# Kernel optimization log

Measured on AMD Instinct MI355X. Metric: run time of the kernel, lower is better.

## Reference

```python
import jax, jax.numpy as jnp
import numpy as np

L, B, D = 2048, 8, 1024
EPS = 1e-5


def setup_inputs() -> dict:
    key = jax.random.key(0)
    k1, k2 = jax.random.split(key)
    x = jax.random.normal(k1, (L, B, D), dtype=jnp.float32)
    c = jnp.zeros((B, D), dtype=jnp.float32)
    # w_ufr: Linear(D, 3D); weight init normal(std=0.001), bias zero except
    # the reset-gate third which is filled with 2.0 (per the torch init).
    W = jax.random.normal(k2, (3 * D, D), dtype=jnp.float32) * 0.001
    b = jnp.zeros((3 * D,), dtype=jnp.float32).at[2 * D:].set(2.0)
    gamma = jnp.ones((D,), dtype=jnp.float32)
    beta = jnp.zeros((D,), dtype=jnp.float32)
    return {"x": x, "c": c, "W": W, "b": b, "gamma": gamma, "beta": beta}


def _layernorm(x, gamma, beta):
    mu = jnp.mean(x, axis=-1, keepdims=True)
    var = jnp.var(x, axis=-1, keepdims=True)
    return (x - mu) * jax.lax.rsqrt(var + EPS) * gamma + beta


def reference(x, c, W, b, gamma, beta):
    residual = x
    x_norm = _layernorm(x, gamma, beta)            # [L,B,D]
    ufr = jnp.einsum('lbd,ed->lbe', x_norm, W) + b  # [L,B,3D]
    u, f, r = jnp.split(ufr, 3, axis=-1)
    f_gate = jax.nn.sigmoid(f)
    r_gate = jax.nn.sigmoid(r)

    def step(c_prev, fu):
        f_t, u_t = fu
        c_t = f_t * c_prev + (1.0 - f_t) * u_t
        return c_t, c_t

    last_c, c_stack = jax.lax.scan(step, c, (f_gate, u))  # c_stack: [L,B,D]
    hs = r_gate * jnp.tanh(c_stack) + (1.0 - r_gate) * x_norm
    # dropout is identity in eval mode
    return residual + hs, last_c
```

## Files before the change

### kernel.cpp

```cpp
#include <hip/hip_runtime.h>
#include <hip/hip_bf16.h>

#define L_DIM 2048
#define B_DIM 8
#define D_DIM 1024
#define M_DIM (L_DIM * B_DIM)
#define N_DIM (3 * D_DIM)
#define K_DIM D_DIM
#define BD (B_DIM * D_DIM)
#define NCHUNK 64
#define CLEN (L_DIM / NCHUNK)

typedef __attribute__((ext_vector_type(8))) __bf16 bf16x8;
typedef __attribute__((ext_vector_type(4))) __bf16 bf16x4;
typedef __attribute__((ext_vector_type(4))) float f32x4;

#define GLOAD_LDS16(g, l)                                        \
  __builtin_amdgcn_global_load_lds(                              \
      (const __attribute__((address_space(1))) void*)(g),        \
      (__attribute__((address_space(3))) void*)(l), 16, 0, 0)

__device__ __forceinline__ float sigmoidf_(float v) {
  return 1.0f / (1.0f + __expf(-v));
}

__global__ __launch_bounds__(256) void ln_kernel(
    const float* __restrict__ x, const float* __restrict__ gamma,
    const float* __restrict__ beta, __bf16* __restrict__ xn,
    float* __restrict__ muA, float* __restrict__ rsA) {
  const int row = blockIdx.x;
  const int tid = threadIdx.x;
  const float4 v = ((const float4*)(x + (size_t)row * D_DIM))[tid];
  float s  = v.x + v.y + v.z + v.w;
  float ss = v.x * v.x + v.y * v.y + v.z * v.z + v.w * v.w;
  #pragma unroll
  for (int off = 32; off > 0; off >>= 1) {
    s  += __shfl_xor(s, off);
    ss += __shfl_xor(ss, off);
  }
  __shared__ float sb[8];
  const int wid = tid >> 6, lane = tid & 63;
  if (lane == 0) { sb[wid] = s; sb[4 + wid] = ss; }
  __syncthreads();
  const float tot  = sb[0] + sb[1] + sb[2] + sb[3];
  const float tot2 = sb[4] + sb[5] + sb[6] + sb[7];
  const float mu  = tot * (1.0f / D_DIM);
  const float var = tot2 * (1.0f / D_DIM) - mu * mu;
  const float rstd = rsqrtf(var + 1e-5f);
  if (tid == 0) { muA[row] = mu; rsA[row] = rstd; }
  const float4 g  = ((const float4*)gamma)[tid];
  const float4 bt = ((const float4*)beta)[tid];
  bf16x4 o;
  o[0] = (__bf16)((v.x - mu) * rstd * g.x + bt.x);
  o[1] = (__bf16)((v.y - mu) * rstd * g.y + bt.y);
  o[2] = (__bf16)((v.z - mu) * rstd * g.z + bt.z);
  o[3] = (__bf16)((v.w - mu) * rstd * g.w + bt.w);
  ((bf16x4*)(xn + (size_t)row * D_DIM))[tid] = o;
}

__global__ __launch_bounds__(256) void wconv_kernel(
    const float* __restrict__ W, __bf16* __restrict__ Wb) {
  const size_t i = ((size_t)blockIdx.x * 256 + threadIdx.x) * 4;
  const float4 v = *(const float4*)(W + i);
  bf16x4 o;
  o[0] = (__bf16)v.x; o[1] = (__bf16)v.y; o[2] = (__bf16)v.z; o[3] = (__bf16)v.w;
  *(bf16x4*)(Wb + i) = o;
}

__global__ __launch_bounds__(256) void gemm_kernel(
    const __bf16* __restrict__ A,
    const __bf16* __restrict__ Bm,
    const float* __restrict__ bias,
    __bf16* __restrict__ U, __bf16* __restrict__ FG, __bf16* __restrict__ RG) {
  __shared__ __bf16 lds[17408];
  const int tid = threadIdx.x;
  const int lane = tid & 63;
  const int wid = tid >> 6;
  const int wm = wid >> 1;
  const int wc = wid & 1;

  const int bid0 = blockIdx.x;
  const int bid = (bid0 & 7) * 384 + (bid0 >> 3);
  const int bm = bid / 24, bn = bid % 24;

  const int srow  = tid >> 3;
  const int sslot = (tid & 7) ^ (srow & 7);
  const __bf16* aSrc = A + (size_t)(bm * 128 + srow) * K_DIM + sslot * 8;
  const __bf16* bSrc = Bm + (size_t)(bn * 128 + srow) * K_DIM + sslot * 8;

  const int fr = lane & 15, fk = lane >> 4;
  const int swzbase = fk ^ (fr & 7);
  auto rdA = [&](int kk, int m) {
    return *(const bf16x8*)(lds + (wm * 64 + m * 16 + fr) * 64 +
                            ((kk * 4) ^ swzbase) * 8);
  };
  auto rdB = [&](int kk, int n) {
    return *(const bf16x8*)(lds + 8192 + (wc * 64 + n * 16 + fr) * 64 +
                            ((kk * 4) ^ swzbase) * 8);
  };

  f32x4 acc[4][4] = {};

  #pragma unroll 1
  for (int kt = 0; kt < 16; ++kt) {
    __syncthreads();
    #pragma unroll
    for (int i = 0; i < 4; ++i) {
      GLOAD_LDS16(aSrc + (size_t)(32 * i) * K_DIM + kt * 64,
                  lds + (tid + 256 * i) * 8);
      GLOAD_LDS16(bSrc + (size_t)(32 * i) * K_DIM + kt * 64,
                  lds + 8192 + (tid + 256 * i) * 8);
    }
    __syncthreads();

    #pragma unroll
    for (int kk = 0; kk < 2; ++kk) {
      bf16x8 a[4], b[4];
      #pragma unroll
      for (int m = 0; m < 4; ++m) a[m] = rdA(kk, m);
      #pragma unroll
      for (int n = 0; n < 4; ++n) b[n] = rdB(kk, n);
      __builtin_amdgcn_s_setprio(1);
      #pragma unroll
      for (int m = 0; m < 4; ++m)
        #pragma unroll
        for (int n = 0; n < 4; ++n)
          acc[m][n] = __builtin_amdgcn_mfma_f32_16x16x32_bf16(
              a[m], b[n], acc[m][n], 0, 0, 0);
      __builtin_amdgcn_s_setprio(0);
    }
  }

  const int seg = bn >> 3;
  __bf16* outb = (seg == 0) ? U : ((seg == 1) ? FG : RG);
  const int segcol0 = (bn & 7) * 128;

  float bv[4];
  #pragma unroll
  for (int n = 0; n < 4; ++n)
    bv[n] = bias[seg * 1024 + segcol0 + wc * 64 + n * 16 + fr];

  __syncthreads();
  #pragma unroll
  for (int m = 0; m < 4; ++m)
    #pragma unroll
    for (int n = 0; n < 4; ++n)
      #pragma unroll
      for (int j = 0; j < 4; ++j) {
        float v = acc[m][n][j] + bv[n];
        if (seg != 0) v = sigmoidf_(v);
        lds[(wm * 64 + m * 16 + fk * 4 + j) * 136 + wc * 64 + n * 16 + fr] =
            (__bf16)v;
      }
  __syncthreads();
  const int lrow = tid >> 4;
  const int chunk = tid & 15;
  #pragma unroll
  for (int it = 0; it < 8; ++it) {
    const int r = it * 16 + lrow;
    const bf16x8 val = *(const bf16x8*)(lds + r * 136 + chunk * 8);
    const size_t grow = (size_t)(bm * 128 + r);
    *(bf16x8*)(outb + grow * D_DIM + segcol0 + chunk * 8) = val;
  }
}

__global__ __launch_bounds__(256) void scanA_kernel(
    const __bf16* __restrict__ fg, const __bf16* __restrict__ u,
    float* __restrict__ av) {
  const int ci = blockIdx.x;
  const int t8 = blockIdx.y * 256 + threadIdx.x;
  const int bd0 = t8 * 8;
  float a[8], v[8];
  #pragma unroll
  for (int j = 0; j < 8; ++j) { a[j] = 1.0f; v[j] = 0.0f; }
  const size_t base = (size_t)ci * CLEN * BD + bd0;
  #pragma unroll 4
  for (int i = 0; i < CLEN; ++i) {
    const size_t idx = base + (size_t)i * BD;
    const bf16x8 fv = *(const bf16x8*)(fg + idx);
    const bf16x8 uv = *(const bf16x8*)(u + idx);
    #pragma unroll
    for (int j = 0; j < 8; ++j) {
      const float f = (float)fv[j];
      a[j] *= f;
      v[j] = f * v[j] + (1.0f - f) * (float)uv[j];
    }
  }
  float4* avA = (float4*)(av + (size_t)ci * BD + bd0);
  float4* avV = (float4*)(av + (size_t)NCHUNK * BD + (size_t)ci * BD + bd0);
  avA[0] = make_float4(a[0], a[1], a[2], a[3]);
  avA[1] = make_float4(a[4], a[5], a[6], a[7]);
  avV[0] = make_float4(v[0], v[1], v[2], v[3]);
  avV[1] = make_float4(v[4], v[5], v[6], v[7]);
}

__global__ __launch_bounds__(256) void scanB_kernel(
    const float* __restrict__ av, const float* __restrict__ c0,
    float* __restrict__ carries, float* __restrict__ out1) {
  const int bd = blockIdx.x * 256 + threadIdx.x;
  float c = c0[bd];
  #pragma unroll 8
  for (int ci = 0; ci < NCHUNK; ++ci) {
    carries[(size_t)ci * BD + bd] = c;
    c = av[(size_t)ci * BD + bd] * c + av[(size_t)NCHUNK * BD + (size_t)ci * BD + bd];
  }
  out1[bd] = c;
}

__global__ __launch_bounds__(256) void scanC_kernel(
    const __bf16* __restrict__ fg, const __bf16* __restrict__ u,
    const __bf16* __restrict__ rg, const float* __restrict__ x,
    const float* __restrict__ muA, const float* __restrict__ rsA,
    const float* __restrict__ gamma, const float* __restrict__ beta,
    const float* __restrict__ carries, float* __restrict__ out0) {
  const int ci = blockIdx.x;
  const int t8 = blockIdx.y * 256 + threadIdx.x;
  const int bd0 = t8 * 8;
  const int b = bd0 >> 10;
  const int d0 = bd0 & 1023;

  float g[8], be[8], c[8];
  #pragma unroll
  for (int j = 0; j < 8; ++j) { g[j] = gamma[d0 + j]; be[j] = beta[d0 + j]; }
  {
    const float4* cp = (const float4*)(carries + (size_t)ci * BD + bd0);
    const float4 c0v = cp[0], c1v = cp[1];
    c[0] = c0v.x; c[1] = c0v.y; c[2] = c0v.z; c[3] = c0v.w;
    c[4] = c1v.x; c[5] = c1v.y; c[6] = c1v.z; c[7] = c1v.w;
  }

  const size_t base = (size_t)ci * CLEN * BD + bd0;
  #pragma unroll 2
  for (int i = 0; i < CLEN; ++i) {
    const size_t idx = base + (size_t)i * BD;
    const int row = (ci * CLEN + i) * B_DIM + b;
    const float mu = muA[row], rs = rsA[row];
    const bf16x8 fv = *(const bf16x8*)(fg + idx);
    const bf16x8 uv = *(const bf16x8*)(u + idx);
    const bf16x8 rv = *(const bf16x8*)(rg + idx);
    const float4* xp = (const float4*)(x + idx);
    const float4 x0 = xp[0], x1 = xp[1];
    const float xs[8] = {x0.x, x0.y, x0.z, x0.w, x1.x, x1.y, x1.z, x1.w};
    float os[8];
    #pragma unroll
    for (int j = 0; j < 8; ++j) {
      const float f = (float)fv[j];
      c[j] = f * c[j] + (1.0f - f) * (float)uv[j];
      const float r = (float)rv[j];
      const float xn = (xs[j] - mu) * rs * g[j] + be[j];
      const float hs = r * tanhf(c[j]) + (1.0f - r) * xn;
      os[j] = xs[j] + hs;
    }
    float4* op = (float4*)(out0 + idx);
    op[0] = make_float4(os[0], os[1], os[2], os[3]);
    op[1] = make_float4(os[4], os[5], os[6], os[7]);
  }
}

extern "C" void kernel_launch(void* const* d_in, const int* in_sizes, int n_in,
                              void* d_out, int out_size, void* d_ws,
                              size_t ws_size, hipStream_t stream) {
  const float* x     = (const float*)d_in[0];
  const float* c0    = (const float*)d_in[1];
  const float* W     = (const float*)d_in[2];
  const float* bias  = (const float*)d_in[3];
  const float* gamma = (const float*)d_in[4];
  const float* beta  = (const float*)d_in[5];

  float* out0 = (float*)d_out;
  float* out1 = out0 + (size_t)M_DIM * D_DIM;

  char* ws = (char*)d_ws;
  __bf16* xn = (__bf16*)(ws + 0);
  __bf16* Wb = (__bf16*)(ws + 33554432);
  __bf16* U  = (__bf16*)(ws + 39845888);
  __bf16* FG = (__bf16*)(ws + 73400320);
  __bf16* RG = (__bf16*)(ws + 106954752);
  float* av      = (float*)(ws + 140509184);
  float* carries = (float*)(ws + 144703488);
  float* muA     = (float*)(ws + 146800640);
  float* rsA     = (float*)(ws + 146866176);

  ln_kernel<<<M_DIM, 256, 0, stream>>>(x, gamma, beta, xn, muA, rsA);
  wconv_kernel<<<(N_DIM * K_DIM / 4) / 256, 256, 0, stream>>>(W, Wb);
  gemm_kernel<<<(M_DIM / 128) * (N_DIM / 128), 256, 0, stream>>>(
      xn, Wb, bias, U, FG, RG);
  scanA_kernel<<<dim3(NCHUNK, BD / 8 / 256), 256, 0, stream>>>(FG, U, av);
  scanB_kernel<<<BD / 256, 256, 0, stream>>>(av, c0, carries, out1);
  scanC_kernel<<<dim3(NCHUNK, BD / 8 / 256), 256, 0, stream>>>(
      FG, U, RG, x, muA, rsA, gamma, beta, carries, out0);
}
```

Measured before the change: 216.4 us.

## Replace GEMM with 256x256-tile, 8-wave, double-buffered pipelined kernel

Measured after the change: 226.8 us. 1.05x slower.

```diff
diff --git a/kernel.cpp b/kernel.cpp
--- a/kernel.cpp
+++ b/kernel.cpp
@@ -67,100 +67,166 @@
   *(bf16x4*)(Wb + i) = o;
 }
 
-__global__ __launch_bounds__(256) void gemm_kernel(
+#define VMCNT(n) asm volatile("s_waitcnt vmcnt(" #n ")" ::: "memory")
+#define BAR __builtin_amdgcn_s_barrier
+
+__global__ __launch_bounds__(512) void gemm256_kernel(
     const __bf16* __restrict__ A,
     const __bf16* __restrict__ Bm,
     const float* __restrict__ bias,
     __bf16* __restrict__ U, __bf16* __restrict__ FG, __bf16* __restrict__ RG) {
-  __shared__ __bf16 lds[17408];
+  __shared__ __bf16 lds[65536];
   const int tid = threadIdx.x;
   const int lane = tid & 63;
   const int wid = tid >> 6;
-  const int wm = wid >> 1;
-  const int wc = wid & 1;
+  const int wm = wid >> 2;
+  const int wn = wid & 3;
 
   const int bid0 = blockIdx.x;
-  const int bid = (bid0 & 7) * 384 + (bid0 >> 3);
-  const int bm = bid / 24, bn = bid % 24;
-
-  const int srow  = tid >> 3;
-  const int sslot = (tid & 7) ^ (srow & 7);
-  const __bf16* aSrc = A + (size_t)(bm * 128 + srow) * K_DIM + sslot * 8;
-  const __bf16* bSrc = Bm + (size_t)(bn * 128 + srow) * K_DIM + sslot * 8;
+  const int bid = (bid0 & 7) * 96 + (bid0 >> 3);
+  const int bm = bid / 12, bn = bid % 12;
+
+  const int srow  = tid >> 2;
+  const int sslot = (tid & 3) ^ ((srow >> 1) & 3);
+
+  auto stageA = [&](int t, int kh) {
+    const __bf16* gs = A + (size_t)(bm * 256 + srow) * K_DIM + t * 64 +
+                       kh * 32 + sslot * 8;
+    __bf16* ld = lds + (t & 1) * 32768 + kh * 8192 + tid * 8;
+    GLOAD_LDS16(gs, ld);
+    GLOAD_LDS16(gs + (size_t)128 * K_DIM, ld + 4096);
+  };
+  auto stageB = [&](int t, int kh) {
+    const __bf16* gs = Bm + (size_t)(bn * 256 + srow) * K_DIM + t * 64 +
+                       kh * 32 + sslot * 8;
+    __bf16* ld = lds + (t & 1) * 32768 + 16384 + kh * 8192 + tid * 8;
+    GLOAD_LDS16(gs, ld);
+    GLOAD_LDS16(gs + (size_t)128 * K_DIM, ld + 4096);
+  };
 
   const int fr = lane & 15, fk = lane >> 4;
-  const int swzbase = fk ^ (fr & 7);
-  auto rdA = [&](int kk, int m) {
-    return *(const bf16x8*)(lds + (wm * 64 + m * 16 + fr) * 64 +
-                            ((kk * 4) ^ swzbase) * 8);
-  };
-  auto rdB = [&](int kk, int n) {
-    return *(const bf16x8*)(lds + 8192 + (wc * 64 + n * 16 + fr) * 64 +
-                            ((kk * 4) ^ swzbase) * 8);
-  };
-
-  f32x4 acc[4][4] = {};
+  const int swz = fk ^ ((fr >> 1) & 3);
+  auto rdA = [&](int buf, int m, int kk) {
+    const int row = wm * 128 + m * 16 + fr;
+    return *(const bf16x8*)(lds + buf * 32768 + kk * 8192 + row * 32 +
+                            swz * 8);
+  };
+  auto rdB = [&](int buf, int n, int kk) {
+    const int row = wn * 64 + n * 16 + fr;
+    return *(const bf16x8*)(lds + buf * 32768 + 16384 + kk * 8192 + row * 32 +
+                            swz * 8);
+  };
+
+  f32x4 acc[8][4] = {};
+
+  stageA(0, 0); stageB(0, 0); stageA(0, 1); stageB(0, 1);
+  stageA(1, 0); stageB(1, 0);
+  VMCNT(4);
+  BAR();
+
+  auto tileBody = [&](int t, int buf) {
+    bf16x8 a[4], b[4];
+    #pragma unroll
+    for (int m = 0; m < 4; ++m) a[m] = rdA(buf, m, 0);
+    #pragma unroll
+    for (int n = 0; n < 4; ++n) b[n] = rdB(buf, n, 0);
+    if (t < 15) stageA(t + 1, 1);
+    BAR();
+    __builtin_amdgcn_s_setprio(1);
+    #pragma unroll
+    for (int m = 0; m < 4; ++m)
+      #pragma unroll
+      for (int n = 0; n < 4; ++n)
+        acc[m][n] = __builtin_amdgcn_mfma_f32_16x16x32_bf16(a[m], b[n],
+                                                            acc[m][n], 0, 0, 0);
+    __builtin_amdgcn_s_setprio(0);
+    BAR();
+    #pragma unroll
+    for (int m = 0; m < 4; ++m) a[m] = rdA(buf, m + 4, 0);
+    if (t < 15) stageB(t + 1, 1);
+    BAR();
+    __builtin_amdgcn_s_setprio(1);
+    #pragma unroll
+    for (int m = 0; m < 4; ++m)
+      #pragma unroll
+      for (int n = 0; n < 4; ++n)
+        acc[m + 4][n] = __builtin_amdgcn_mfma_f32_16x16x32_bf16(
+            a[m], b[n], acc[m + 4][n], 0, 0, 0);
+    __builtin_amdgcn_s_setprio(0);
+    BAR();
+    #pragma unroll
+    for (int m = 0; m < 4; ++m) a[m] = rdA(buf, m, 1);
+    #pragma unroll
+    for (int n = 0; n < 4; ++n) b[n] = rdB(buf, n, 1);
+    if (t < 14) stageA(t + 2, 0);
+    BAR();
+    __builtin_amdgcn_s_setprio(1);
+    #pragma unroll
+    for (int m = 0; m < 4; ++m)
+      #pragma unroll
+      for (int n = 0; n < 4; ++n)
+        acc[m][n] = __builtin_amdgcn_mfma_f32_16x16x32_bf16(a[m], b[n],
+                                                            acc[m][n], 0, 0, 0);
+    __builtin_amdgcn_s_setprio(0);
+    BAR();
+    #pragma unroll
+    for (int m = 0; m < 4; ++m) a[m] = rdA(buf, m + 4, 1);
+    if (t < 14) stageB(t + 2, 0);
+    BAR();
+    __builtin_amdgcn_s_setprio(1);
+    #pragma unroll
+    for (int m = 0; m < 4; ++m)
+      #pragma unroll
+      for (int n = 0; n < 4; ++n)
+        acc[m + 4][n] = __builtin_amdgcn_mfma_f32_16x16x32_bf16(
+            a[m], b[n], acc[m + 4][n], 0, 0, 0);
+    __builtin_amdgcn_s_setprio(0);
+    if (t <= 13) { VMCNT(4); }
+    else if (t == 14) { VMCNT(0); }
+    BAR();
+  };
 
   #pragma unroll 1
-  for (int kt = 0; kt < 16; ++kt) {
-    __syncthreads();
-    #pragma unroll
-    for (int i = 0; i < 4; ++i) {
-      GLOAD_LDS16(aSrc + (size_t)(32 * i) * K_DIM + kt * 64,
-                  lds + (tid + 256 * i) * 8);
-      GLOAD_LDS16(bSrc + (size_t)(32 * i) * K_DIM + kt * 64,
-                  lds + 8192 + (tid + 256 * i) * 8);
-    }
-    __syncthreads();
-
-    #pragma unroll
-    for (int kk = 0; kk < 2; ++kk) {
-      bf16x8 a[4], b[4];
-      #pragma unroll
-      for (int m = 0; m < 4; ++m) a[m] = rdA(kk, m);
-      #pragma unroll
-      for (int n = 0; n < 4; ++n) b[n] = rdB(kk, n);
-      __builtin_amdgcn_s_setprio(1);
-      #pragma unroll
-      for (int m = 0; m < 4; ++m)
-        #pragma unroll
-        for (int n = 0; n < 4; ++n)
-          acc[m][n] = __builtin_amdgcn_mfma_f32_16x16x32_bf16(
-              a[m], b[n], acc[m][n], 0, 0, 0);
-      __builtin_amdgcn_s_setprio(0);
-    }
-  }
-
-  const int seg = bn >> 3;
+  for (int i = 0; i < 8; ++i) {
+    tileBody(2 * i, 0);
+    tileBody(2 * i + 1, 1);
+  }
+
+  const int seg = bn >> 2;
   __bf16* outb = (seg == 0) ? U : ((seg == 1) ? FG : RG);
-  const int segcol0 = (bn & 7) * 128;
+  const int segcol0 = (bn & 3) * 256;
 
   float bv[4];
   #pragma unroll
   for (int n = 0; n < 4; ++n)
-    bv[n] = bias[seg * 1024 + segcol0 + wc * 64 + n * 16 + fr];
-
-  __syncthreads();
-  #pragma unroll
-  for (int m = 0; m < 4; ++m)
-    #pragma unroll
-    for (int n = 0; n < 4; ++n)
-      #pragma unroll
-      for (int j = 0; j < 4; ++j) {
-        float v = acc[m][n][j] + bv[n];
-        if (seg != 0) v = sigmoidf_(v);
-        lds[(wm * 64 + m * 16 + fk * 4 + j) * 136 + wc * 64 + n * 16 + fr] =
-            (__bf16)v;
-      }
-  __syncthreads();
-  const int lrow = tid >> 4;
-  const int chunk = tid & 15;
-  #pragma unroll
-  for (int it = 0; it < 8; ++it) {
-    const int r = it * 16 + lrow;
-    const bf16x8 val = *(const bf16x8*)(lds + r * 136 + chunk * 8);
-    const size_t grow = (size_t)(bm * 128 + r);
-    *(bf16x8*)(outb + grow * D_DIM + segcol0 + chunk * 8) = val;
+    bv[n] = bias[seg * 1024 + segcol0 + wn * 64 + n * 16 + fr];
+
+  const int lrow = tid >> 5;
+  const int chunk = tid & 31;
+  #pragma unroll 1
+  for (int h = 0; h < 2; ++h) {
+    __syncthreads();
+    if (wm == h) {
+      #pragma unroll
+      for (int m = 0; m < 8; ++m)
+        #pragma unroll
+        for (int n = 0; n < 4; ++n)
+          #pragma unroll
+          for (int j = 0; j < 4; ++j) {
+            float v = acc[m][n][j] + bv[n];
+            if (seg != 0) v = sigmoidf_(v);
+            lds[(m * 16 + fk * 4 + j) * 264 + wn * 64 + n * 16 + fr] =
+                (__bf16)v;
+          }
+    }
+    __syncthreads();
+    #pragma unroll
+    for (int it = 0; it < 8; ++it) {
+      const int r = it * 16 + lrow;
+      const bf16x8 val = *(const bf16x8*)(lds + r * 264 + chunk * 8);
+      const size_t grow = (size_t)(bm * 256 + h * 128 + r);
+      *(bf16x8*)(outb + grow * D_DIM + segcol0 + chunk * 8) = val;
+    }
   }
 }
 
@@ -283,7 +349,7 @@
 
   ln_kernel<<<M_DIM, 256, 0, stream>>>(x, gamma, beta, xn, muA, rsA);
   wconv_kernel<<<(N_DIM * K_DIM / 4) / 256, 256, 0, stream>>>(W, Wb);
-  gemm_kernel<<<(M_DIM / 128) * (N_DIM / 128), 256, 0, stream>>>(
+  gemm256_kernel<<<(M_DIM / 256) * (N_DIM / 256), 512, 0, stream>>>(
       xn, Wb, bias, U, FG, RG);
   scanA_kernel<<<dim3(NCHUNK, BD / 8 / 256), 256, 0, stream>>>(FG, U, av);
   scanB_kernel<<<BD / 256, 256, 0, stream>>>(av, c0, carries, out1);
```
